# Performance work log

Measured on AMD Instinct MI355X. Metric: run time of the kernel, lower is better.

## Reference

```python
import jax, jax.numpy as jnp
import numpy as np

BS, N, L, H, E, W, K = 32, 512, 4096, 256, 64, 8, 9
NE = 2048            # edges per graph
CIN = H + 2 * E + W  # pc1 input channels
CS = K // 2          # center slice start
LC = L - (K - 1)     # valid-conv output length
EPS = 1e-5


def setup_inputs() -> dict:
    key = jax.random.key(0)
    ks = jax.random.split(key, 12)
    s = 0.05
    d = {}
    d["x"] = jax.random.normal(ks[0], (BS, N, H), jnp.float32)
    d["edge_feat"] = jax.random.normal(ks[1], (BS, NE, E), jnp.float32)
    d["walk_nodes"] = jax.random.randint(ks[2], (BS, L), 0, N - 1)
    d["walk_edges"] = jax.random.randint(ks[3], (BS, L - 1), 0, NE)
    d["encodings"] = jax.random.normal(ks[4], (BS, W, L), jnp.float32)
    d["ln_g"] = jnp.ones((H,), jnp.float32)
    d["ln_b"] = jnp.zeros((H,), jnp.float32)
    d["pc1_w"] = jax.random.normal(ks[5], (2 * H, CIN), jnp.float32) * s
    d["pc1_b"] = jnp.zeros((2 * H,), jnp.float32)
    d["dc_w"] = jax.random.normal(ks[6], (H, K), jnp.float32) * s
    d["bn_g"] = jnp.ones((H,), jnp.float32)
    d["bn_b"] = jnp.zeros((H,), jnp.float32)
    d["pc2_w"] = jax.random.normal(ks[7], (H, H), jnp.float32) * s
    d["pc2_b"] = jnp.zeros((H,), jnp.float32)
    d["mlp_w1"] = jax.random.normal(ks[8], (H, H), jnp.float32) * s
    d["bn2_g"] = jnp.ones((H,), jnp.float32)
    d["bn2_b"] = jnp.zeros((H,), jnp.float32)
    d["mlp_w2"] = jax.random.normal(ks[9], (H, H), jnp.float32) * s
    return d


def reference(x, edge_feat, walk_nodes, walk_edges, encodings,
              ln_g, ln_b, pc1_w, pc1_b, dc_w, bn_g, bn_b,
              pc2_w, pc2_b, mlp_w1, bn2_g, bn2_b, mlp_w2):
    # LayerNorm over hidden dim
    mu = x.mean(-1, keepdims=True)
    var = x.var(-1, keepdims=True)
    xn = (x - mu) * jax.lax.rsqrt(var + EPS) * ln_g + ln_b

    vn = xn[:, 0]  # [BS, H]

    # gather walk node features: x[batch, walk_nodes+1] -> [BS, H, L]
    xg = jnp.take_along_axis(xn, (walk_nodes + 1)[:, :, None], axis=1)
    xg = xg.transpose(0, 2, 1)

    # gather walk edge features -> [BS, E, L-1], pad to in/out channels of len L
    we = jnp.take_along_axis(edge_feat, walk_edges[:, :, None], axis=1).transpose(0, 2, 1)
    pad = jnp.zeros((BS, E, 1), xg.dtype)
    we_i = jnp.concatenate([pad, we], axis=2)
    we_o = jnp.concatenate([we, pad], axis=2)

    h = jnp.concatenate([xg, we_i, we_o, encodings], axis=1)  # [BS, CIN, L]

    # pointwise conv 1 + GLU
    h = jnp.einsum('oc,bcl->bol', pc1_w, h) + pc1_b[None, :, None]
    out, gate = jnp.split(h, 2, axis=1)
    h = out * jax.nn.sigmoid(gate)  # [BS, H, L]

    # depthwise conv, VALID -> [BS, H, LC]
    h = jax.lax.conv_general_dilated(
        h, dc_w[:, None, :], window_strides=(1,), padding='VALID',
        feature_group_count=H, dimension_numbers=('NCH', 'OIH', 'NCH'))

    # BatchNorm1d (training mode, biased var over batch+length)
    m = h.mean((0, 2))
    v = h.var((0, 2))
    h = (h - m[None, :, None]) * jax.lax.rsqrt(v + EPS)[None, :, None] \
        * bn_g[None, :, None] + bn_b[None, :, None]

    # Swish + pointwise conv 2
    h = h * jax.nn.sigmoid(h)
    h = jnp.einsum('oc,bcl->bol', pc2_w, h) + pc2_b[None, :, None]
    h = h.transpose(0, 2, 1)  # [BS, LC, H]

    # scatter_mean over center nodes into n-1 real-node slots
    center = jax.lax.dynamic_slice_in_dim(walk_nodes, CS, LC, axis=1)  # [BS, LC]
    flat_idx = (center + jnp.arange(BS, dtype=center.dtype)[:, None] * (N - 1)).reshape(-1)
    sums = jax.ops.segment_sum(h.reshape(BS * LC, H), flat_idx, num_segments=BS * (N - 1))
    cnt = jax.ops.segment_sum(jnp.ones((BS * LC,), h.dtype), flat_idx, num_segments=BS * (N - 1))
    node_out = (sums / jnp.maximum(cnt, 1.0)[:, None]).reshape(BS, N - 1, H)

    # virtual node MLP: Linear -> BN -> ReLU -> Linear
    z = (vn + node_out.sum(1)) @ mlp_w1.T
    m2 = z.mean(0)
    v2 = z.var(0)
    z = (z - m2) * jax.lax.rsqrt(v2 + EPS) * bn2_g + bn2_b
    z = jax.nn.relu(z) @ mlp_w2.T
    vn_out = z[:, None]  # [BS, 1, H]

    return jnp.concatenate([vn_out, node_out + vn_out], axis=1)  # [BS, N, H]
```

## Files before the change

kernel.cpp:

```cpp
#include <hip/hip_runtime.h>
#include <hip/hip_bf16.h>

typedef __hip_bfloat16 bf16;
typedef __attribute__((ext_vector_type(8))) short short8v;
typedef __attribute__((ext_vector_type(4))) float f32x4;

#define BS 32
#define NN 512
#define LL 4096
#define HH 256
#define EE 64
#define WW 8
#define KK 9
#define NE 2048
#define CIN 392
#define KP 416
#define FS 424
#define FS2 264
#define LC 4088
#define NM1 511
#define CR 128
#define K2M 64
#define K5M 64

__device__ __forceinline__ float b2f(bf16 v) { return __bfloat162float(v); }
__device__ __forceinline__ float bfr(unsigned short u) {
    union { unsigned int i; float f; } cv; cv.i = ((unsigned int)u) << 16; return cv.f;
}
__device__ __forceinline__ unsigned short f2b(float v) {
    return __builtin_bit_cast(unsigned short, __float2bfloat16(v));
}
__device__ __forceinline__ unsigned int pack2(float a, float b) {
    return (unsigned int)f2b(a) | ((unsigned int)f2b(b) << 16);
}
__device__ __forceinline__ float sigm(float x) {
    return __builtin_amdgcn_rcpf(1.f + __expf(-x));
}

__global__ void k0_all(const float* __restrict__ pc1w, const float* __restrict__ pc2w,
                       const float* __restrict__ edge, unsigned short* __restrict__ wb,
                       unsigned short* __restrict__ w2b, unsigned short* __restrict__ eb) {
    size_t i = (size_t)blockIdx.x * 256 + threadIdx.x;
    eb[i] = f2b(edge[i]);
    if (i < (size_t)512 * KP) {
        int row = (int)(i / KP), c = (int)(i % KP);
        wb[i] = (c < CIN) ? f2b(pc1w[(size_t)row * CIN + c]) : 0;
    }
    if (i < (size_t)HH * HH) w2b[i] = f2b(pc2w[i]);
}

__global__ void k1_layernorm(const float* __restrict__ x, const float* __restrict__ ln_g,
                             const float* __restrict__ ln_b, unsigned short* __restrict__ xnb,
                             float* __restrict__ acc) {
    int b = blockIdx.y, n = blockIdx.x, t = threadIdx.x;
    size_t base = ((size_t)(b * NN + n)) * HH;
    float v = x[base + t];
    __shared__ float s1[4], s2[4], mv[2];
    float a = v, q = v * v;
    #pragma unroll
    for (int o = 32; o > 0; o >>= 1) { a += __shfl_down(a, o, 64); q += __shfl_down(q, o, 64); }
    if ((t & 63) == 0) { s1[t >> 6] = a; s2[t >> 6] = q; }
    __syncthreads();
    if (t == 0) {
        float sa = s1[0] + s1[1] + s1[2] + s1[3];
        float sq = s2[0] + s2[1] + s2[2] + s2[3];
        float mean = sa * (1.0f / 256.0f);
        float var = sq * (1.0f / 256.0f) - mean * mean;
        mv[0] = mean; mv[1] = rsqrtf(var + 1e-5f);
    }
    __syncthreads();
    float outv = (v - mv[0]) * mv[1] * ln_g[t] + ln_b[t];
    xnb[base + t] = f2b(outv);
    if (n == 0) acc[b * HH + t] = outv;
}

__global__ void kb_all(const int* __restrict__ wn, int* __restrict__ offs,
                       int* __restrict__ bins) {
    __shared__ int cnt[NM1];
    __shared__ int cur[NM1];
    __shared__ int ps[256];
    int b = blockIdx.x, t = threadIdx.x;
    for (int i = t; i < NM1; i += 256) cnt[i] = 0;
    __syncthreads();
    for (int l = t; l < LC; l += 256)
        atomicAdd(&cnt[wn[b * LL + l + (KK / 2)]], 1);
    __syncthreads();
    int c0 = (2 * t < NM1)     ? cnt[2 * t]     : 0;
    int c1 = (2 * t + 1 < NM1) ? cnt[2 * t + 1] : 0;
    int pair = c0 + c1;
    ps[t] = pair;
    __syncthreads();
    for (int o = 1; o < 256; o <<= 1) {
        int add = (t >= o) ? ps[t - o] : 0;
        __syncthreads();
        ps[t] += add;
        __syncthreads();
    }
    int ex = ps[t] - pair;
    offs[b * 512 + 2 * t] = ex;
    offs[b * 512 + 2 * t + 1] = ex + c0;
    if (2 * t < NM1)     cur[2 * t]     = ex;
    if (2 * t + 1 < NM1) cur[2 * t + 1] = ex + c0;
    __syncthreads();
    for (int l = t; l < LC; l += 256) {
        int c = wn[b * LL + l + (KK / 2)];
        int slot = atomicAdd(&cur[c], 1);
        bins[b * LC + slot] = l;
    }
}

__global__ void __launch_bounds__(256, 2)
k2_mfma(const unsigned short* __restrict__ xnb, const unsigned short* __restrict__ edgeb,
        const int* __restrict__ wn, const int* __restrict__ we,
        const float* __restrict__ enc, const unsigned short* __restrict__ wb,
        const float* __restrict__ pc1_b, unsigned short* __restrict__ h1) {
    __shared__ __align__(16) unsigned short smem[K2M * FS];
    __shared__ int rown[K2M], ein[K2M], eout[K2M];
    int id = blockIdx.x;
    int xcd = id & 7, s = id >> 3;
    int b = xcd * 4 + (s >> 6);
    int l0 = (s & 63) * K2M;
    int t = threadIdx.x;
    int lane = t & 63, wv = t >> 6;
    int l15 = lane & 15, lr = (lane >> 4) & 3, koff = lr * 8;
    int c0 = wv * 64;
    const unsigned short* wrO = wb + ((size_t)(c0 + l15)) * KP + koff;
    const unsigned short* wrG = wb + ((size_t)(HH + c0 + l15)) * KP + koff;

    short8v bo0[4], bg0[4], bo1[4], bg1[4];
    #pragma unroll
    for (int n = 0; n < 4; ++n) {
        bo0[n] = *(const short8v*)(wrO + (size_t)n * 16 * KP);
        bg0[n] = *(const short8v*)(wrG + (size_t)n * 16 * KP);
    }

    if (t < K2M) {
        int l = l0 + t;
        rown[t] = wn[b * LL + l] + 1;
        ein[t]  = (l > 0)      ? we[b * (LL - 1) + l - 1] : -1;
        eout[t] = (l < LL - 1) ? we[b * (LL - 1) + l]     : -1;
    }
    __syncthreads();

    for (int i = t; i < K2M * 32; i += 256) {
        int r = i >> 5, c = (i & 31) * 8;
        *(uint4*)&smem[r * FS + c] =
            *(const uint4*)(xnb + ((size_t)(b * NN + rown[r])) * HH + c);
    }
    for (int i = t; i < K2M * 16; i += 256) {
        int r = i >> 4, q = i & 15;
        int idx = (q < 8) ? ein[r] : eout[r];
        uint4 v = {0u, 0u, 0u, 0u};
        if (idx >= 0)
            v = *(const uint4*)(edgeb + ((size_t)(b * NE + idx)) * EE + (q & 7) * 8);
        *(uint4*)&smem[r * FS + HH + q * 8] = v;
    }
    for (int i = t; i < K2M * 5; i += 256) {
        int r = i / 5, q = i % 5;
        uint4 v = {0u, 0u, 0u, 0u};
        if (q == 0) {
            const float* ep = enc + (size_t)b * WW * LL + (l0 + r);
            v.x = pack2(ep[0], ep[LL]);          v.y = pack2(ep[2 * LL], ep[3 * LL]);
            v.z = pack2(ep[4 * LL], ep[5 * LL]); v.w = pack2(ep[6 * LL], ep[7 * LL]);
        }
        *(uint4*)&smem[r * FS + (HH + 2 * EE) + q * 8] = v;
    }
    __syncthreads();

    f32x4 acc[4][8];
    #pragma unroll
    for (int m = 0; m < 4; ++m)
        #pragma unroll
        for (int n = 0; n < 8; ++n) acc[m][n] = (f32x4){0.f, 0.f, 0.f, 0.f};

    const unsigned short* arow = &smem[l15 * FS + koff];

    #pragma unroll 1
    for (int p = 0; p < 6; ++p) {
        int kk = 2 * p;
        #pragma unroll
        for (int n = 0; n < 4; ++n) {
            bo1[n] = *(const short8v*)(wrO + (size_t)n * 16 * KP + (kk + 1) * 32);
            bg1[n] = *(const short8v*)(wrG + (size_t)n * 16 * KP + (kk + 1) * 32);
        }
        {
            short8v a[4];
            #pragma unroll
            for (int m = 0; m < 4; ++m)
                a[m] = *(const short8v*)(arow + (size_t)m * 16 * FS + kk * 32);
            #pragma unroll
            for (int m = 0; m < 4; ++m)
                #pragma unroll
                for (int n = 0; n < 4; ++n) {
                    acc[m][n]     = __builtin_amdgcn_mfma_f32_16x16x32_bf16(a[m], bo0[n], acc[m][n], 0, 0, 0);
                    acc[m][n + 4] = __builtin_amdgcn_mfma_f32_16x16x32_bf16(a[m], bg0[n], acc[m][n + 4], 0, 0, 0);
                }
        }
        #pragma unroll
        for (int n = 0; n < 4; ++n) {
            bo0[n] = *(const short8v*)(wrO + (size_t)n * 16 * KP + (kk + 2) * 32);
            bg0[n] = *(const short8v*)(wrG + (size_t)n * 16 * KP + (kk + 2) * 32);
        }
        {
            short8v a[4];
            #pragma unroll
            for (int m = 0; m < 4; ++m)
                a[m] = *(const short8v*)(arow + (size_t)m * 16 * FS + (kk + 1) * 32);
            #pragma unroll
            for (int m = 0; m < 4; ++m)
                #pragma unroll
                for (int n = 0; n < 4; ++n) {
                    acc[m][n]     = __builtin_amdgcn_mfma_f32_16x16x32_bf16(a[m], bo1[n], acc[m][n], 0, 0, 0);
                    acc[m][n + 4] = __builtin_amdgcn_mfma_f32_16x16x32_bf16(a[m], bg1[n], acc[m][n + 4], 0, 0, 0);
                }
        }
    }
    {
        short8v a[4];
        #pragma unroll
        for (int m = 0; m < 4; ++m)
            a[m] = *(const short8v*)(arow + (size_t)m * 16 * FS + 12 * 32);
        #pragma unroll
        for (int m = 0; m < 4; ++m)
            #pragma unroll
            for (int n = 0; n < 4; ++n) {
                acc[m][n]     = __builtin_amdgcn_mfma_f32_16x16x32_bf16(a[m], bo0[n], acc[m][n], 0, 0, 0);
                acc[m][n + 4] = __builtin_amdgcn_mfma_f32_16x16x32_bf16(a[m], bg0[n], acc[m][n + 4], 0, 0, 0);
            }
    }

    float biasO[4], biasG[4];
    #pragma unroll
    for (int n = 0; n < 4; ++n) {
        biasO[n] = pc1_b[c0 + n * 16 + l15];
        biasG[n] = pc1_b[HH + c0 + n * 16 + l15];
    }

    __syncthreads();
    unsigned short* glu = smem;
    int cb = c0 + l15;
    #pragma unroll
    for (int m = 0; m < 4; ++m)
        #pragma unroll
        for (int n = 0; n < 4; ++n)
            #pragma unroll
            for (int r = 0; r < 4; ++r) {
                int pos = m * 16 + lr * 4 + r;
                float o = acc[m][n][r] + biasO[n];
                float g = acc[m][n + 4][r] + biasG[n];
                glu[pos * FS2 + cb + n * 16] = f2b(o * sigm(g));
            }
    __syncthreads();
    for (int i = t; i < K2M * 32; i += 256) {
        int r = i >> 5, c = (i & 31) * 8;
        *(uint4*)(h1 + ((size_t)(b * LL) + l0 + r) * HH + c) = *(const uint4*)&glu[r * FS2 + c];
    }
}

__global__ void k3f_conv_stats(const unsigned short* __restrict__ h1, const float* __restrict__ dc_w,
                               unsigned short* __restrict__ h2, float* __restrict__ bnsum,
                               float* __restrict__ bnsumsq) {
    __shared__ float sr[4][HH], qr[4][HH];
    int b = blockIdx.y, l0 = blockIdx.x * CR, t = threadIdx.x;
    int g = t >> 6, c4 = (t & 63) * 4;
    int rows_all = min(CR, LC - l0);
    int r0 = g * (CR / 4);
    int r1 = min(r0 + CR / 4, rows_all);

    float wk[4][KK];
    #pragma unroll
    for (int j = 0; j < 4; ++j)
        #pragma unroll
        for (int k = 0; k < KK; ++k) wk[j][k] = dc_w[(c4 + j) * KK + k];

    float s[4] = {0.f, 0.f, 0.f, 0.f}, q[4] = {0.f, 0.f, 0.f, 0.f};
    if (r0 < r1) {
        const unsigned short* src = h1 + ((size_t)b * LL + l0 + r0) * HH + c4;
        float w[KK][4];
        float nxt[4];
        #pragma unroll
        for (int k = 0; k < KK - 1; ++k) {
            uint2 v = *(const uint2*)(src + (size_t)k * HH);
            w[k][0] = bfr((unsigned short)(v.x & 0xffffu)); w[k][1] = bfr((unsigned short)(v.x >> 16));
            w[k][2] = bfr((unsigned short)(v.y & 0xffffu)); w[k][3] = bfr((unsigned short)(v.y >> 16));
        }
        {
            uint2 v = *(const uint2*)(src + (size_t)(KK - 1) * HH);
            nxt[0] = bfr((unsigned short)(v.x & 0xffffu)); nxt[1] = bfr((unsigned short)(v.x >> 16));
            nxt[2] = bfr((unsigned short)(v.y & 0xffffu)); nxt[3] = bfr((unsigned short)(v.y >> 16));
        }
        for (int i = r0; i < r1; ++i) {
            #pragma unroll
            for (int j = 0; j < 4; ++j) w[KK - 1][j] = nxt[j];
            if (i + 1 < r1) {
                uint2 v = *(const uint2*)(src + (size_t)(i - r0 + KK) * HH);
                nxt[0] = bfr((unsigned short)(v.x & 0xffffu)); nxt[1] = bfr((unsigned short)(v.x >> 16));
                nxt[2] = bfr((unsigned short)(v.y & 0xffffu)); nxt[3] = bfr((unsigned short)(v.y >> 16));
            }
            float o[4];
            #pragma unroll
            for (int j = 0; j < 4; ++j) {
                float v = 0.f;
                #pragma unroll
                for (int k = 0; k < KK; ++k) v += w[k][j] * wk[j][k];
                o[j] = v;
                s[j] += v; q[j] += v * v;
            }
            uint2 ov;
            ov.x = pack2(o[0], o[1]); ov.y = pack2(o[2], o[3]);
            *(uint2*)(h2 + ((size_t)b * LC + l0 + i) * HH + c4) = ov;
            #pragma unroll
            for (int k = 0; k < KK - 1; ++k)
                #pragma unroll
                for (int j = 0; j < 4; ++j) w[k][j] = w[k + 1][j];
        }
    }
    #pragma unroll
    for (int j = 0; j < 4; ++j) { sr[g][c4 + j] = s[j]; qr[g][c4 + j] = q[j]; }
    __syncthreads();
    float ss = sr[0][t] + sr[1][t] + sr[2][t] + sr[3][t];
    float qq = qr[0][t] + qr[1][t] + qr[2][t] + qr[3][t];
    atomicAdd(&bnsum[t], ss);
    atomicAdd(&bnsumsq[t], qq);
}

__global__ void __launch_bounds__(256, 3)
k5_mfma(const unsigned short* __restrict__ h2, const float* __restrict__ bnsum,
        const float* __restrict__ bnsumsq, const float* __restrict__ bn_g,
        const float* __restrict__ bn_b, const unsigned short* __restrict__ w2b,
        const float* __restrict__ pc2_b, unsigned short* __restrict__ h3) {
    __shared__ __align__(16) unsigned short smem[K5M * FS2];
    __shared__ float scl[HH], shl[HH];
    int b = blockIdx.y, l0 = blockIdx.x * K5M, t = threadIdx.x;
    int lane = t & 63, wv = t >> 6;
    int l15 = lane & 15, lr = (lane >> 4) & 3, koff = lr * 8;
    int c0 = wv * 64;
    const unsigned short* wrow = w2b + ((size_t)(c0 + l15)) * HH + koff;

    short8v b0[4], b1[4];
    #pragma unroll
    for (int n = 0; n < 4; ++n) b0[n] = *(const short8v*)(wrow + (size_t)n * 16 * HH);

    {
        const float M = (float)(BS * LC);
        float mean = bnsum[t] / M;
        float var = bnsumsq[t] / M - mean * mean;
        float rstd = rsqrtf(var + 1e-5f);
        float sc = rstd * bn_g[t];
        scl[t] = sc;
        shl[t] = bn_b[t] - mean * sc;
    }
    __syncthreads();

    for (int i = t; i < K5M * 32; i += 256) {
        int r = i >> 5, c = (i & 31) * 8;
        int l = l0 + r;
        uint4 out = {0u, 0u, 0u, 0u};
        if (l < LC) {
            uint4 v = *(const uint4*)(h2 + ((size_t)b * LC + l) * HH + c);
            unsigned int vv[4] = {v.x, v.y, v.z, v.w};
            unsigned int oo[4];
            #pragma unroll
            for (int j = 0; j < 4; ++j) {
                float f0 = bfr((unsigned short)(vv[j] & 0xffffu));
                float f1 = bfr((unsigned short)(vv[j] >> 16));
                float a0 = f0 * scl[c + 2 * j]     + shl[c + 2 * j];
                float a1 = f1 * scl[c + 2 * j + 1] + shl[c + 2 * j + 1];
                a0 = a0 * sigm(a0);
                a1 = a1 * sigm(a1);
                oo[j] = pack2(a0, a1);
            }
            out.x = oo[0]; out.y = oo[1]; out.z = oo[2]; out.w = oo[3];
        }
        *(uint4*)&smem[r * FS2 + c] = out;
    }
    __syncthreads();

    f32x4 acc[4][4];
    #pragma unroll
    for (int m = 0; m < 4; ++m)
        #pragma unroll
        for (int n = 0; n < 4; ++n) acc[m][n] = (f32x4){0.f, 0.f, 0.f, 0.f};

    const unsigned short* arow = &smem[l15 * FS2 + koff];

    #pragma unroll 1
    for (int p = 0; p < 4; ++p) {
        int kk = 2 * p;
        #pragma unroll
        for (int n = 0; n < 4; ++n)
            b1[n] = *(const short8v*)(wrow + (size_t)n * 16 * HH + (kk + 1) * 32);
        {
            short8v a[4];
            #pragma unroll
            for (int m = 0; m < 4; ++m)
                a[m] = *(const short8v*)(arow + (size_t)m * 16 * FS2 + kk * 32);
            #pragma unroll
            for (int m = 0; m < 4; ++m)
                #pragma unroll
                for (int n = 0; n < 4; ++n)
                    acc[m][n] = __builtin_amdgcn_mfma_f32_16x16x32_bf16(a[m], b0[n], acc[m][n], 0, 0, 0);
        }
        if (p < 3) {
            #pragma unroll
            for (int n = 0; n < 4; ++n)
                b0[n] = *(const short8v*)(wrow + (size_t)n * 16 * HH + (kk + 2) * 32);
        }
        {
            short8v a[4];
            #pragma unroll
            for (int m = 0; m < 4; ++m)
                a[m] = *(const short8v*)(arow + (size_t)m * 16 * FS2 + (kk + 1) * 32);
            #pragma unroll
            for (int m = 0; m < 4; ++m)
                #pragma unroll
                for (int n = 0; n < 4; ++n)
                    acc[m][n] = __builtin_amdgcn_mfma_f32_16x16x32_bf16(a[m], b1[n], acc[m][n], 0, 0, 0);
        }
    }

    int chb = c0 + l15;
    float bias[4];
    #pragma unroll
    for (int n = 0; n < 4; ++n) bias[n] = pc2_b[chb + n * 16];

    __syncthreads();
    #pragma unroll
    for (int m = 0; m < 4; ++m)
        #pragma unroll
        for (int n = 0; n < 4; ++n)
            #pragma unroll
            for (int r = 0; r < 4; ++r) {
                int pos = m * 16 + lr * 4 + r;
                smem[pos * FS2 + chb + n * 16] = f2b(acc[m][n][r] + bias[n]);
            }
    __syncthreads();
    for (int i = t; i < K5M * 32; i += 256) {
        int r = i >> 5, c = (i & 31) * 8;
        int l = l0 + r;
        if (l < LC)
            *(uint4*)(h3 + ((size_t)b * LC + l) * HH + c) = *(const uint4*)&smem[r * FS2 + c];
    }
}

__global__ void k6_gather(const unsigned short* __restrict__ h3, const int* __restrict__ offs,
                          const int* __restrict__ bins, float* __restrict__ node_out) {
    __shared__ float red[8][HH];
    int bn = blockIdx.x;
    int b = bn / NM1, n = bn % NM1, t = threadIdx.x;
    int s = offs[b * 512 + n], e = offs[b * 512 + n + 1];
    int g = t >> 5, lane32 = t & 31;
    int c8 = lane32 * 8;
    float sum[8] = {0.f, 0.f, 0.f, 0.f, 0.f, 0.f, 0.f, 0.f};
    for (int i = s + g; i < e; i += 8) {
        int l = bins[b * LC + i];
        uint4 v = *(const uint4*)(h3 + ((size_t)b * LC + l) * HH + c8);
        sum[0] += bfr((unsigned short)(v.x & 0xffffu)); sum[1] += bfr((unsigned short)(v.x >> 16));
        sum[2] += bfr((unsigned short)(v.y & 0xffffu)); sum[3] += bfr((unsigned short)(v.y >> 16));
        sum[4] += bfr((unsigned short)(v.z & 0xffffu)); sum[5] += bfr((unsigned short)(v.z >> 16));
        sum[6] += bfr((unsigned short)(v.w & 0xffffu)); sum[7] += bfr((unsigned short)(v.w >> 16));
    }
    #pragma unroll
    for (int j = 0; j < 8; ++j) red[g][c8 + j] = sum[j];
    __syncthreads();
    float tot = red[0][t] + red[1][t] + red[2][t] + red[3][t]
              + red[4][t] + red[5][t] + red[6][t] + red[7][t];
    float inv = 1.f / (float)max(e - s, 1);
    node_out[(size_t)bn * HH + t] = tot * inv;
}

__global__ void k6b_accsum(const float* __restrict__ node_out, float* __restrict__ acc) {
    int b = blockIdx.y, g = blockIdx.x, t = threadIdx.x;
    int n0 = g * 32, n1 = min(n0 + 32, NM1);
    float s = 0.f;
    for (int n = n0; n < n1; ++n) s += node_out[((size_t)b * NM1 + n) * HH + t];
    atomicAdd(&acc[b * HH + t], s);
}

__global__ void k7_mlp1(const float* __restrict__ acc, const float* __restrict__ w1,
                        float* __restrict__ z) {
    int b = blockIdx.x, t = threadIdx.x;
    __shared__ float a[HH];
    a[t] = acc[b * HH + t];
    __syncthreads();
    const float* w = w1 + (size_t)t * HH;
    float s = 0.f;
    for (int c = 0; c < HH; ++c) s += w[c] * a[c];
    z[b * HH + t] = s;
}

__global__ void k9_mlp2(const float* __restrict__ z, const float* __restrict__ g2,
                        const float* __restrict__ b2v, const float* __restrict__ w2,
                        float* __restrict__ vnout) {
    int b = blockIdx.x, t = threadIdx.x;
    __shared__ float a[HH];
    float m = 0.f, q = 0.f;
    for (int bb = 0; bb < BS; ++bb) {
        float v = z[bb * HH + t];
        m += v; q += v * v;
    }
    m *= (1.0f / BS);
    q = q * (1.0f / BS) - m * m;
    float rstd = rsqrtf(q + 1e-5f);
    float sc = rstd * g2[t];
    float sh = b2v[t] - m * sc;
    a[t] = fmaxf(z[b * HH + t] * sc + sh, 0.f);
    __syncthreads();
    const float* w = w2 + (size_t)t * HH;
    float s = 0.f;
    for (int c = 0; c < HH; ++c) s += w[c] * a[c];
    vnout[b * HH + t] = s;
}

__global__ void k10_out(const float* __restrict__ vnout, const float* __restrict__ node_out,
                        float* __restrict__ out) {
    int bn = blockIdx.x;
    int b = bn >> 9, n = bn & (NN - 1), t = threadIdx.x;
    float vo = vnout[b * HH + t];
    float v = (n == 0) ? vo : node_out[((size_t)b * NM1 + (n - 1)) * HH + t] + vo;
    out[(size_t)bn * HH + t] = v;
}

extern "C" void kernel_launch(void* const* d_in, const int* in_sizes, int n_in,
                              void* d_out, int out_size, void* d_ws, size_t ws_size,
                              hipStream_t stream) {
    const float* x     = (const float*)d_in[0];
    const float* edge  = (const float*)d_in[1];
    const int*   wn    = (const int*)d_in[2];
    const int*   we    = (const int*)d_in[3];
    const float* enc   = (const float*)d_in[4];
    const float* ln_g  = (const float*)d_in[5];
    const float* ln_b  = (const float*)d_in[6];
    const float* pc1_w = (const float*)d_in[7];
    const float* pc1_b = (const float*)d_in[8];
    const float* dc_w  = (const float*)d_in[9];
    const float* bn_g  = (const float*)d_in[10];
    const float* bn_b  = (const float*)d_in[11];
    const float* pc2_w = (const float*)d_in[12];
    const float* pc2_b = (const float*)d_in[13];
    const float* w1    = (const float*)d_in[14];
    const float* g2    = (const float*)d_in[15];
    const float* b2v   = (const float*)d_in[16];
    const float* w2    = (const float*)d_in[17];

    char* ws = (char*)d_ws;
    unsigned short* xnb   = (unsigned short*)(ws + 0);
    unsigned short* wbf   = (unsigned short*)(ws + 8388608);
    unsigned short* h1    = (unsigned short*)(ws + 8814592);
    unsigned short* h3    = h1;
    unsigned short* h2    = (unsigned short*)(ws + 75923456);
    float* node_out = (float*)(ws + 142901248);
    unsigned short* edgeb = (unsigned short*)(ws + 142901248);
    float* bnsum   = (float*)(ws + 159711104);
    float* bnsumsq = (float*)(ws + 159712128);
    float* acc     = (float*)(ws + 159713152);
    float* z       = (float*)(ws + 159747968);
    float* vnout   = (float*)(ws + 159780736);
    unsigned short* w2b = (unsigned short*)(ws + 159813504);
    int*   offs    = (int*)(ws + 159944576);
    int*   bins    = (int*)(ws + 160075520);

    hipMemsetAsync(ws + 159711104, 0, 2048, stream);

    k0_all<<<(BS * NE * EE) / 256, 256, 0, stream>>>(pc1_w, pc2_w, edge, wbf, w2b, edgeb);
    k1_layernorm<<<dim3(NN, BS), 256, 0, stream>>>(x, ln_g, ln_b, xnb, acc);
    kb_all<<<BS, 256, 0, stream>>>(wn, offs, bins);
    k2_mfma<<<(LL / K2M) * BS, 256, 0, stream>>>(xnb, edgeb, wn, we, enc, wbf, pc1_b, h1);
    k3f_conv_stats<<<dim3((LC + CR - 1) / CR, BS), 256, 0, stream>>>(h1, dc_w, h2, bnsum, bnsumsq);
    k5_mfma<<<dim3((LC + K5M - 1) / K5M, BS), 256, 0, stream>>>(h2, bnsum, bnsumsq, bn_g, bn_b, w2b, pc2_b, h3);
    k6_gather<<<BS * NM1, 256, 0, stream>>>(h3, offs, bins, node_out);
    k6b_accsum<<<dim3(16, BS), 256, 0, stream>>>(node_out, acc);
    k7_mlp1<<<BS, 256, 0, stream>>>(acc, w1, z);
    k9_mlp2<<<BS, 256, 0, stream>>>(z, g2, b2v, w2, vnout);
    k10_out<<<BS * NN, 256, 0, stream>>>(vnout, node_out, (float*)d_out);
}
```

Before: 266.4 us.

## Recompute depthwise conv in pc2 kernel instead of storing h2; XCD-aware block mapping

The stats kernel now only accumulates BatchNorm sums and no longer writes the depthwise-conv output h2. The pc2 MFMA kernel recomputes the 9-tap conv from h1, applies BN and Swish, and feeds the result straight into shared memory. This removes a full bf16 write and read of h2 at the cost of computing the conv twice. Block indices in the conv, pc2 and gather kernels are also remapped so that each of the 8 XCDs handles a contiguous group of 4 batches, aiming at better L2 locality.

```diff
diff --git a/kernel.cpp b/kernel.cpp
--- a/kernel.cpp
+++ b/kernel.cpp
@@ -257,11 +257,14 @@
     }
 }
 
-__global__ void k3f_conv_stats(const unsigned short* __restrict__ h1, const float* __restrict__ dc_w,
-                               unsigned short* __restrict__ h2, float* __restrict__ bnsum,
-                               float* __restrict__ bnsumsq) {
+__global__ void k3s_stats(const unsigned short* __restrict__ h1, const float* __restrict__ dc_w,
+                          float* __restrict__ bnsum, float* __restrict__ bnsumsq) {
     __shared__ float sr[4][HH], qr[4][HH];
-    int b = blockIdx.y, l0 = blockIdx.x * CR, t = threadIdx.x;
+    int id = blockIdx.x;
+    int xcd = id & 7, s5 = id >> 3;
+    int b = xcd * 4 + (s5 >> 5);
+    int l0 = (s5 & 31) * CR;
+    int t = threadIdx.x;
     int g = t >> 6, c4 = (t & 63) * 4;
     int rows_all = min(CR, LC - l0);
     int r0 = g * (CR / 4);
@@ -297,18 +300,13 @@
                 nxt[0] = bfr((unsigned short)(v.x & 0xffffu)); nxt[1] = bfr((unsigned short)(v.x >> 16));
                 nxt[2] = bfr((unsigned short)(v.y & 0xffffu)); nxt[3] = bfr((unsigned short)(v.y >> 16));
             }
-            float o[4];
             #pragma unroll
             for (int j = 0; j < 4; ++j) {
                 float v = 0.f;
                 #pragma unroll
                 for (int k = 0; k < KK; ++k) v += w[k][j] * wk[j][k];
-                o[j] = v;
                 s[j] += v; q[j] += v * v;
             }
-            uint2 ov;
-            ov.x = pack2(o[0], o[1]); ov.y = pack2(o[2], o[3]);
-            *(uint2*)(h2 + ((size_t)b * LC + l0 + i) * HH + c4) = ov;
             #pragma unroll
             for (int k = 0; k < KK - 1; ++k)
                 #pragma unroll
@@ -325,13 +323,18 @@
 }
 
 __global__ void __launch_bounds__(256, 3)
-k5_mfma(const unsigned short* __restrict__ h2, const float* __restrict__ bnsum,
-        const float* __restrict__ bnsumsq, const float* __restrict__ bn_g,
-        const float* __restrict__ bn_b, const unsigned short* __restrict__ w2b,
-        const float* __restrict__ pc2_b, unsigned short* __restrict__ h3) {
+k5_mfma(const unsigned short* __restrict__ h1, const float* __restrict__ dc_w,
+        const float* __restrict__ bnsum, const float* __restrict__ bnsumsq,
+        const float* __restrict__ bn_g, const float* __restrict__ bn_b,
+        const unsigned short* __restrict__ w2b, const float* __restrict__ pc2_b,
+        unsigned short* __restrict__ h3) {
     __shared__ __align__(16) unsigned short smem[K5M * FS2];
     __shared__ float scl[HH], shl[HH];
-    int b = blockIdx.y, l0 = blockIdx.x * K5M, t = threadIdx.x;
+    int id = blockIdx.x;
+    int xcd = id & 7, s = id >> 3;
+    int b = xcd * 4 + (s >> 6);
+    int l0 = (s & 63) * K5M;
+    int t = threadIdx.x;
     int lane = t & 63, wv = t >> 6;
     int l15 = lane & 15, lr = (lane >> 4) & 3, koff = lr * 8;
     int c0 = wv * 64;
@@ -352,27 +355,58 @@
     }
     __syncthreads();
 
-    for (int i = t; i < K5M * 32; i += 256) {
-        int r = i >> 5, c = (i & 31) * 8;
-        int l = l0 + r;
-        uint4 out = {0u, 0u, 0u, 0u};
-        if (l < LC) {
-            uint4 v = *(const uint4*)(h2 + ((size_t)b * LC + l) * HH + c);
-            unsigned int vv[4] = {v.x, v.y, v.z, v.w};
-            unsigned int oo[4];
-            #pragma unroll
-            for (int j = 0; j < 4; ++j) {
-                float f0 = bfr((unsigned short)(vv[j] & 0xffffu));
-                float f1 = bfr((unsigned short)(vv[j] >> 16));
-                float a0 = f0 * scl[c + 2 * j]     + shl[c + 2 * j];
-                float a1 = f1 * scl[c + 2 * j + 1] + shl[c + 2 * j + 1];
-                a0 = a0 * sigm(a0);
-                a1 = a1 * sigm(a1);
-                oo[j] = pack2(a0, a1);
+    {
+        int g = t >> 6, c4 = (t & 63) * 4;
+        int rbase = l0 + g * 16;
+        float wk[4][KK];
+        #pragma unroll
+        for (int j = 0; j < 4; ++j)
+            #pragma unroll
+            for (int k = 0; k < KK; ++k) wk[j][k] = dc_w[(c4 + j) * KK + k];
+        const unsigned short* hb = h1 + (size_t)b * LL * HH + c4;
+        float w[KK][4], nxt[4];
+        #pragma unroll
+        for (int k = 0; k < KK - 1; ++k) {
+            int rr = min(rbase + k, LL - 1);
+            uint2 v = *(const uint2*)(hb + (size_t)rr * HH);
+            w[k][0] = bfr((unsigned short)(v.x & 0xffffu)); w[k][1] = bfr((unsigned short)(v.x >> 16));
+            w[k][2] = bfr((unsigned short)(v.y & 0xffffu)); w[k][3] = bfr((unsigned short)(v.y >> 16));
+        }
+        {
+            int rr = min(rbase + KK - 1, LL - 1);
+            uint2 v = *(const uint2*)(hb + (size_t)rr * HH);
+            nxt[0] = bfr((unsigned short)(v.x & 0xffffu)); nxt[1] = bfr((unsigned short)(v.x >> 16));
+            nxt[2] = bfr((unsigned short)(v.y & 0xffffu)); nxt[3] = bfr((unsigned short)(v.y >> 16));
+        }
+        for (int i = 0; i < 16; ++i) {
+            #pragma unroll
+            for (int j = 0; j < 4; ++j) w[KK - 1][j] = nxt[j];
+            if (i + 1 < 16) {
+                int rr = min(rbase + i + KK, LL - 1);
+                uint2 v = *(const uint2*)(hb + (size_t)rr * HH);
+                nxt[0] = bfr((unsigned short)(v.x & 0xffffu)); nxt[1] = bfr((unsigned short)(v.x >> 16));
+                nxt[2] = bfr((unsigned short)(v.y & 0xffffu)); nxt[3] = bfr((unsigned short)(v.y >> 16));
             }
-            out.x = oo[0]; out.y = oo[1]; out.z = oo[2]; out.w = oo[3];
-        }
-        *(uint4*)&smem[r * FS2 + c] = out;
+            int lrow = rbase + i;
+            uint2 ov = {0u, 0u};
+            if (lrow < LC) {
+                float a[4];
+                #pragma unroll
+                for (int j = 0; j < 4; ++j) {
+                    float v = 0.f;
+                    #pragma unroll
+                    for (int k = 0; k < KK; ++k) v += w[k][j] * wk[j][k];
+                    float x = v * scl[c4 + j] + shl[c4 + j];
+                    a[j] = x * sigm(x);
+                }
+                ov.x = pack2(a[0], a[1]); ov.y = pack2(a[2], a[3]);
+            }
+            *(uint2*)&smem[(g * 16 + i) * FS2 + c4] = ov;
+            #pragma unroll
+            for (int k = 0; k < KK - 1; ++k)
+                #pragma unroll
+                for (int j = 0; j < 4; ++j) w[k][j] = w[k + 1][j];
+        }
     }
     __syncthreads();
 
@@ -446,8 +480,11 @@
 __global__ void k6_gather(const unsigned short* __restrict__ h3, const int* __restrict__ offs,
                           const int* __restrict__ bins, float* __restrict__ node_out) {
     __shared__ float red[8][HH];
-    int bn = blockIdx.x;
-    int b = bn / NM1, n = bn % NM1, t = threadIdx.x;
+    int id = blockIdx.x;
+    int xcd = id & 7, sx = id >> 3;
+    int b = xcd * 4 + sx / NM1;
+    int n = sx % NM1;
+    int t = threadIdx.x;
     int s = offs[b * 512 + n], e = offs[b * 512 + n + 1];
     int g = t >> 5, lane32 = t & 31;
     int c8 = lane32 * 8;
@@ -466,7 +503,7 @@
     float tot = red[0][t] + red[1][t] + red[2][t] + red[3][t]
               + red[4][t] + red[5][t] + red[6][t] + red[7][t];
     float inv = 1.f / (float)max(e - s, 1);
-    node_out[(size_t)bn * HH + t] = tot * inv;
+    node_out[((size_t)b * NM1 + n) * HH + t] = tot * inv;
 }
 
 __global__ void k6b_accsum(const float* __restrict__ node_out, float* __restrict__ acc) {
@@ -547,8 +584,7 @@
     unsigned short* xnb   = (unsigned short*)(ws + 0);
     unsigned short* wbf   = (unsigned short*)(ws + 8388608);
     unsigned short* h1    = (unsigned short*)(ws + 8814592);
-    unsigned short* h3    = h1;
-    unsigned short* h2    = (unsigned short*)(ws + 75923456);
+    unsigned short* h3    = (unsigned short*)(ws + 75923456);
     float* node_out = (float*)(ws + 142901248);
     unsigned short* edgeb = (unsigned short*)(ws + 142901248);
     float* bnsum   = (float*)(ws + 159711104);
@@ -566,9 +602,9 @@
     k1_layernorm<<<dim3(NN, BS), 256, 0, stream>>>(x, ln_g, ln_b, xnb, acc);
     kb_all<<<BS, 256, 0, stream>>>(wn, offs, bins);
     k2_mfma<<<(LL / K2M) * BS, 256, 0, stream>>>(xnb, edgeb, wn, we, enc, wbf, pc1_b, h1);
-    k3f_conv_stats<<<dim3((LC + CR - 1) / CR, BS), 256, 0, stream>>>(h1, dc_w, h2, bnsum, bnsumsq);
-    k5_mfma<<<dim3((LC + K5M - 1) / K5M, BS), 256, 0, stream>>>(h2, bnsum, bnsumsq, bn_g, bn_b, w2b, pc2_b, h3);
-    k6_gather<<<BS * NM1, 256, 0, stream>>>(h3, offs, bins, node_out);
+    k3s_stats<<<32 * BS, 256, 0, stream>>>(h1, dc_w, bnsum, bnsumsq);
+    k5_mfma<<<(LL / K5M) * BS, 256, 0, stream>>>(h1, dc_w, bnsum, bnsumsq, bn_g, bn_b, w2b, pc2_b, h3);
+    k6_gather<<<8 * (4 * NM1), 256, 0, stream>>>(h3, offs, bins, node_out);
     k6b_accsum<<<dim3(16, BS), 256, 0, stream>>>(node_out, acc);
     k7_mlp1<<<BS, 256, 0, stream>>>(acc, w1, z);
     k9_mlp2<<<BS, 256, 0, stream>>>(z, g2, b2v, w2, vnout);
```

Result: no change. 267.7 us (+0.5%).
